# Kernel tuning notes

Measured on AMD Instinct MI355X. Metric: run time of the kernel, lower is better.

## Reference

```python
import jax, jax.numpy as jnp
import numpy as np

B, S, D, H = 2, 2048, 1024, 16
DK = D // H  # 64

def setup_inputs() -> dict:
    key = jax.random.key(0)
    ks = jax.random.split(key, 8)
    xavier = np.sqrt(6.0 / (D + D))  # xavier_uniform bound for square Linear
    def lin_w(k):
        return jax.random.uniform(k, (D, D), jnp.float32, -xavier, xavier)
    return {
        'Q': jax.random.normal(ks[0], (B, S, D), jnp.float32),
        'length': jax.random.randint(ks[1], (B,), 1, S + 1, jnp.int32),
        'Wq': lin_w(ks[2]), 'bq': jnp.zeros((D,), jnp.float32),
        'Wk': lin_w(ks[3]), 'bk': jnp.zeros((D,), jnp.float32),
        'Wv': lin_w(ks[4]), 'bv': jnp.zeros((D,), jnp.float32),
    }

def reference(Q, length, Wq, bq, Wk, bk, Wv, bv):
    # project and split heads: [B,S,D] -> [B,H,S,DK]
    def heads(x, W, b):
        y = jnp.einsum('bsd,de->bse', x, W) + b
        return y.reshape(B, S, H, DK).transpose(0, 2, 1, 3)
    q = heads(Q, Wq, bq)
    k = heads(Q, Wk, bk)
    v = heads(Q, Wv, bv)
    scores = jnp.einsum('bhqd,bhkd->bhqk', q, k) / np.sqrt(DK)
    scores = jnp.exp(scores)  # NOTE: raw exp, no max-subtraction (faithful)
    # multiplicative key mask: mask[b,k] = k < length[b], broadcast over q,h
    mask = (jnp.arange(S)[None, :] < length[:, None]).astype(scores.dtype)
    scores = scores * mask[:, None, None, :]
    attn = scores / (jnp.sum(scores, axis=-1, keepdims=True) + 1e-8)
    ctx = jnp.einsum('bhqk,bhkd->bhqd', attn, v)
    return ctx.transpose(0, 2, 1, 3).reshape(B, S, D)
```

## Files before the change

### kernel.cpp

```cpp
#include <hip/hip_runtime.h>
#include <hip/hip_bf16.h>

#define B_  2
#define S_  2048
#define D_  1024
#define H_  16
#define DK_ 64
#define M_  (B_ * S_)

typedef short short8 __attribute__((ext_vector_type(8)));
typedef float float4v __attribute__((ext_vector_type(4)));

#define QSCALE 0.18033688011112042f

static __device__ __forceinline__ ushort f32_to_bf16bits(float f) {
    union { __hip_bfloat16 h; ushort u; } cv;
    cv.h = __float2bfloat16(f);
    return cv.u;
}
static __device__ __forceinline__ unsigned pk2(float a, float b) {
    return (unsigned)f32_to_bf16bits(a) | ((unsigned)f32_to_bf16bits(b) << 16);
}

static __device__ __forceinline__ void glds16(const ushort* g, ushort* l) {
    __builtin_amdgcn_global_load_lds(
        (const __attribute__((address_space(1))) unsigned int*)g,
        (__attribute__((address_space(3))) unsigned int*)l, 16, 0, 0);
}

__global__ __launch_bounds__(256) void prep(
    const float* __restrict__ X, const float* __restrict__ W0,
    const float* __restrict__ W1, const float* __restrict__ W2,
    ushort* __restrict__ Xb, ushort* __restrict__ Wt)
{
    const int z = blockIdx.z;
    const int t = threadIdx.x;

    if (z >= 3) {
        const int blk = (z - 3) * 256 + blockIdx.y * 16 + blockIdx.x;
        const int i = blk * 2048 + t * 8;
        float4v a = *(const float4v*)(X + i);
        float4v b = *(const float4v*)(X + i + 4);
        short8 o;
        o[0] = (short)f32_to_bf16bits(a[0]); o[1] = (short)f32_to_bf16bits(a[1]);
        o[2] = (short)f32_to_bf16bits(a[2]); o[3] = (short)f32_to_bf16bits(a[3]);
        o[4] = (short)f32_to_bf16bits(b[0]); o[5] = (short)f32_to_bf16bits(b[1]);
        o[6] = (short)f32_to_bf16bits(b[2]); o[7] = (short)f32_to_bf16bits(b[3]);
        *(short8*)(Xb + i) = o;
        return;
    }

    const float* W = (z == 0) ? W0 : ((z == 1) ? W1 : W2);
    ushort* out = Wt + (size_t)z * D_ * D_;

    __shared__ ushort tile[64 * 72];
    int n0 = blockIdx.x * 64, k0 = blockIdx.y * 64;
    int r = t >> 3, g = t & 7;

    #pragma unroll
    for (int p = 0; p < 2; ++p) {
        int rr = r + p * 32;
        const float* src = W + (size_t)(k0 + rr) * D_ + n0 + g * 8;
        float4v a = *(const float4v*)src;
        float4v b = *(const float4v*)(src + 4);
        short8 o;
        o[0] = (short)f32_to_bf16bits(a[0]); o[1] = (short)f32_to_bf16bits(a[1]);
        o[2] = (short)f32_to_bf16bits(a[2]); o[3] = (short)f32_to_bf16bits(a[3]);
        o[4] = (short)f32_to_bf16bits(b[0]); o[5] = (short)f32_to_bf16bits(b[1]);
        o[6] = (short)f32_to_bf16bits(b[2]); o[7] = (short)f32_to_bf16bits(b[3]);
        *(short8*)&tile[rr * 72 + g * 8] = o;
    }
    __syncthreads();
    #pragma unroll
    for (int p = 0; p < 2; ++p) {
        int rr = r + p * 32;
        short8 v;
        #pragma unroll
        for (int i = 0; i < 8; ++i)
            v[i] = (short)tile[(g * 8 + i) * 72 + rr];
        *(short8*)(out + (size_t)(n0 + rr) * D_ + k0 + g * 8) = v;
    }
}

__global__ __launch_bounds__(256, 3) void proj_gemm(
    const ushort* __restrict__ X,
    const ushort* __restrict__ Wt,
    const float* __restrict__ b0, const float* __restrict__ b1,
    const float* __restrict__ b2,
    const int* __restrict__ length,
    ushort* __restrict__ qkv)
{
    const int z = blockIdx.z;
    const int m0 = blockIdx.x * 64, n0 = blockIdx.y * 128;

    if (z >= 1) {
        const int bidx = m0 >> 11;
        const int s0 = m0 & (S_ - 1);
        if (s0 >= length[bidx]) return;
    }

    const ushort* Wtz  = Wt + (size_t)z * D_ * D_;
    const float* bias = (z == 0) ? b0 : ((z == 1) ? b1 : b2);
    ushort* out = qkv + (size_t)z * M_ * D_;

    __shared__ __align__(16) ushort As[2][64 * 64];
    __shared__ __align__(16) ushort Bs[2][128 * 64];

    const int t = threadIdx.x;
    const int lane = t & 63, wid = t >> 6;
    const int quad = lane >> 4, l16 = lane & 15;
    const int wr = wid >> 1, wc = wid & 1;

    float4v acc[2][4] = {};

    #pragma unroll
    for (int j = 0; j < 2; ++j) {
        const int cid = wid * 128 + j * 64 + lane;
        const int row = cid >> 3;
        const int cl  = (cid & 7) ^ (row & 7);
        glds16(X + (size_t)(m0 + row) * D_ + cl * 8, &As[0][cid * 8]);
    }
    #pragma unroll
    for (int j = 0; j < 4; ++j) {
        const int cid = wid * 256 + j * 64 + lane;
        const int row = cid >> 3;
        const int cl  = (cid & 7) ^ (row & 7);
        glds16(Wtz + (size_t)(n0 + row) * D_ + cl * 8, &Bs[0][cid * 8]);
    }
    __syncthreads();

    for (int kt = 0; kt < 16; ++kt) {
        const int cur = kt & 1, nxt = cur ^ 1;
        if (kt + 1 < 16) {
            const int k0 = (kt + 1) * 64;
            #pragma unroll
            for (int j = 0; j < 2; ++j) {
                const int cid = wid * 128 + j * 64 + lane;
                const int row = cid >> 3;
                const int cl  = (cid & 7) ^ (row & 7);
                glds16(X + (size_t)(m0 + row) * D_ + k0 + cl * 8, &As[nxt][cid * 8]);
            }
            #pragma unroll
            for (int j = 0; j < 4; ++j) {
                const int cid = wid * 256 + j * 64 + lane;
                const int row = cid >> 3;
                const int cl  = (cid & 7) ^ (row & 7);
                glds16(Wtz + (size_t)(n0 + row) * D_ + k0 + cl * 8, &Bs[nxt][cid * 8]);
            }
        }

        #pragma unroll
        for (int ks = 0; ks < 2; ++ks) {
            short8 a[2], bb[4];
            #pragma unroll
            for (int i = 0; i < 2; ++i) {
                const int r = wr * 32 + i * 16 + l16;
                const int ph = (ks * 4 + quad) ^ (r & 7);
                a[i] = *(short8*)&As[cur][r * 64 + ph * 8];
            }
            #pragma unroll
            for (int j = 0; j < 4; ++j) {
                const int r = wc * 64 + j * 16 + l16;
                const int ph = (ks * 4 + quad) ^ (r & 7);
                bb[j] = *(short8*)&Bs[cur][r * 64 + ph * 8];
            }
            #pragma unroll
            for (int i = 0; i < 2; ++i)
                #pragma unroll
                for (int j = 0; j < 4; ++j)
                    acc[i][j] = __builtin_amdgcn_mfma_f32_16x16x32_bf16(
                        a[i], bb[j], acc[i][j], 0, 0, 0);
        }
        __syncthreads();
    }

    const float sc = (z == 0) ? QSCALE : 1.0f;
    #pragma unroll
    for (int j = 0; j < 4; ++j) {
        const int col = n0 + wc * 64 + j * 16 + l16;
        const float bv = bias[col];
        const int h = col >> 6, dk = col & (DK_ - 1);
        #pragma unroll
        for (int i = 0; i < 2; ++i) {
            #pragma unroll
            for (int rr = 0; rr < 4; ++rr) {
                const int row = m0 + wr * 32 + i * 16 + quad * 4 + rr;
                const int bidx = row >> 11;
                const int s = row & (S_ - 1);
                const float v = (acc[i][j][rr] + bv) * sc;
                size_t addr;
                if (z == 2)
                    addr = ((size_t)(bidx * H_ + h) * DK_ + dk) * S_ + s;
                else
                    addr = ((size_t)(bidx * H_ + h) * S_ + s) * DK_ + dk;
                out[addr] = f32_to_bf16bits(v);
            }
        }
    }
}

__global__ __launch_bounds__(256, 3) void attention(
    const ushort* __restrict__ qkv, const int* __restrict__ length,
    float* __restrict__ out)
{
    const int b = blockIdx.z, h = blockIdx.y, q0 = blockIdx.x * 64;
    int len = length[b];
    if (len > S_) len = S_;
    if (len < 1) len = 1;
    const int nkt = (len + 63) >> 6;

    const ushort* qb = qkv + ((size_t)(b * H_ + h) * S_ + q0) * DK_;
    const ushort* kb = qkv + (size_t)M_ * D_ + (size_t)(b * H_ + h) * S_ * DK_;
    const ushort* vb = qkv + (size_t)2 * M_ * D_ + (size_t)(b * H_ + h) * DK_ * S_;

    __shared__ __align__(16) ushort Qs[64 * 64];
    __shared__ __align__(16) ushort Ks[2][64 * 64];
    __shared__ __align__(16) ushort Vs[2][64 * 64];
    __shared__ __align__(16) ushort Ps[64 * 64];

    const int t = threadIdx.x, lane = t & 63, wid = t >> 6;
    const int quad = lane >> 4, l16 = lane & 15;
    const int qrow = wid * 16 + l16;
    const int e8 = (l16 & 7) << 1;

    #pragma unroll
    for (int j = 0; j < 2; ++j) {
        const int cid = wid * 128 + j * 64 + lane;
        const int row = cid >> 3;
        const int cl  = (cid & 7) ^ (row & 7);
        glds16(qb + (size_t)row * DK_ + cl * 8, &Qs[cid * 8]);
        glds16(kb + (size_t)row * DK_ + cl * 8, &Ks[0][cid * 8]);
        glds16(vb + (size_t)row * S_ + cl * 8,  &Vs[0][cid * 8]);
    }
    __syncthreads();

    float4v cacc[4] = {};
    float rs = 0.f;

    for (int kt = 0; kt < nkt; ++kt) {
        const int cur = kt & 1, nxt = cur ^ 1;
        if (kt + 1 < nkt) {
            #pragma unroll
            for (int j = 0; j < 2; ++j) {
                const int cid = wid * 128 + j * 64 + lane;
                const int row = cid >> 3;
                const int cl  = (cid & 7) ^ (row & 7);
                glds16(kb + (size_t)((kt + 1) * 64 + row) * DK_ + cl * 8,
                       &Ks[nxt][cid * 8]);
                glds16(vb + (size_t)row * S_ + (kt + 1) * 64 + cl * 8,
                       &Vs[nxt][cid * 8]);
            }
        }

        float4v sacc[4] = {};
        #pragma unroll
        for (int ks = 0; ks < 2; ++ks) {
            const int phb = (ks * 4 + quad) ^ (l16 & 7);
            short8 bq8 = *(short8*)&Qs[qrow * 64 + phb * 8];
            #pragma unroll
            for (int ct = 0; ct < 4; ++ct) {
                const int krow = ct * 16 + l16;
                const int pha = (ks * 4 + quad) ^ (krow & 7);
                short8 ak = *(short8*)&Ks[cur][krow * 64 + pha * 8];
                sacc[ct] = __builtin_amdgcn_mfma_f32_16x16x32_bf16(
                    ak, bq8, sacc[ct], 0, 0, 0);
            }
        }

        const bool full = ((kt + 1) * 64 <= len);
        #pragma unroll
        for (int ct = 0; ct < 4; ++ct) {
            float v0 = __builtin_amdgcn_exp2f(sacc[ct][0]);
            float v1 = __builtin_amdgcn_exp2f(sacc[ct][1]);
            float v2 = __builtin_amdgcn_exp2f(sacc[ct][2]);
            float v3 = __builtin_amdgcn_exp2f(sacc[ct][3]);
            if (!full) {
                const int kb0 = kt * 64 + ct * 16 + quad * 4;
                v0 = (kb0 + 0 < len) ? v0 : 0.f;
                v1 = (kb0 + 1 < len) ? v1 : 0.f;
                v2 = (kb0 + 2 < len) ? v2 : 0.f;
                v3 = (kb0 + 3 < len) ? v3 : 0.f;
            }
            rs += (v0 + v1) + (v2 + v3);
            uint2 w;
            w.x = pk2(v0, v1);
            w.y = pk2(v2, v3);
            const int c8 = (ct * 4 + quad) ^ e8;
            *(uint2*)&Ps[qrow * 64 + c8 * 4] = w;
        }

        #pragma unroll
        for (int ks = 0; ks < 2; ++ks) {
            const int pp = ((ks * 4 + quad) * 2) ^ e8;
            short8 ap = *(short8*)&Ps[qrow * 64 + pp * 4];
            #pragma unroll
            for (int ct = 0; ct < 4; ++ct) {
                const int vrow = ct * 16 + l16;
                const int phv = (ks * 4 + quad) ^ (vrow & 7);
                short8 vv = *(short8*)&Vs[cur][vrow * 64 + phv * 8];
                cacc[ct] = __builtin_amdgcn_mfma_f32_16x16x32_bf16(
                    ap, vv, cacc[ct], 0, 0, 0);
            }
        }
        __syncthreads();
    }

    rs += __shfl_xor(rs, 16);
    rs += __shfl_xor(rs, 32);

    #pragma unroll
    for (int rr = 0; rr < 4; ++rr) {
        const float rsq = __shfl(rs, quad * 4 + rr, 16);
        const float inv = 1.0f / (rsq + 1e-8f);
        const int q = q0 + wid * 16 + quad * 4 + rr;
        #pragma unroll
        for (int ct = 0; ct < 4; ++ct) {
            const int d = h * 64 + ct * 16 + l16;
            out[((size_t)b * S_ + q) * D_ + d] = cacc[ct][rr] * inv;
        }
    }
}

extern "C" void kernel_launch(void* const* d_in, const int* in_sizes, int n_in,
                              void* d_out, int out_size, void* d_ws, size_t ws_size,
                              hipStream_t stream)
{
    const float* Q   = (const float*)d_in[0];
    const int*   len = (const int*)d_in[1];
    const float* Wq  = (const float*)d_in[2];
    const float* bq  = (const float*)d_in[3];
    const float* Wk  = (const float*)d_in[4];
    const float* bk  = (const float*)d_in[5];
    const float* Wv  = (const float*)d_in[6];
    const float* bv  = (const float*)d_in[7];
    float* out = (float*)d_out;

    ushort* ws  = (ushort*)d_ws;
    ushort* Xb  = ws;
    ushort* Wt  = ws + (size_t)M_ * D_;
    ushort* qkv = Wt + (size_t)3 * D_ * D_;

    dim3 gPr(16, 16, 11);
    prep<<<gPr, 256, 0, stream>>>(Q, Wq, Wk, Wv, Xb, Wt);

    dim3 gP(M_ / 64, D_ / 128, 3);
    proj_gemm<<<gP, 256, 0, stream>>>(Xb, Wt, bq, bk, bv, len, qkv);

    dim3 gA(S_ / 64, H_, B_);
    attention<<<gA, 256, 0, stream>>>(qkv, len, out);
}
```

Before: 167.8 us.

## Fuse Q/K/V projections into one block sharing the X tile

The projection GEMM now computes the Q, K and V outputs in a single block, so each X tile is loaded into shared memory once and reused across all three weight matrices. The grid z dimension is removed, and the K/V work for masked rows is skipped with a per-block flag instead of an early return. In exchange, the double-buffered prefetch pipeline is dropped in favour of synchronous single-buffered loads. The larger B tile and three accumulator sets also raise shared memory and register use, and launch bounds drop to 2 blocks per SM. Blocks past the valid length now do only Q work while the others do triple work, which can cause load imbalance.

```diff
diff --git a/kernel.cpp b/kernel.cpp
--- a/kernel.cpp
+++ b/kernel.cpp
@@ -82,7 +82,7 @@
     }
 }
 
-__global__ __launch_bounds__(256, 3) void proj_gemm(
+__global__ __launch_bounds__(256, 2) void proj_gemm(
     const ushort* __restrict__ X,
     const ushort* __restrict__ Wt,
     const float* __restrict__ b0, const float* __restrict__ b1,
@@ -90,110 +90,109 @@
     const int* __restrict__ length,
     ushort* __restrict__ qkv)
 {
-    const int z = blockIdx.z;
     const int m0 = blockIdx.x * 64, n0 = blockIdx.y * 128;
-
-    if (z >= 1) {
-        const int bidx = m0 >> 11;
-        const int s0 = m0 & (S_ - 1);
-        if (s0 >= length[bidx]) return;
-    }
-
-    const ushort* Wtz  = Wt + (size_t)z * D_ * D_;
-    const float* bias = (z == 0) ? b0 : ((z == 1) ? b1 : b2);
-    ushort* out = qkv + (size_t)z * M_ * D_;
-
-    __shared__ __align__(16) ushort As[2][64 * 64];
-    __shared__ __align__(16) ushort Bs[2][128 * 64];
+    const int bidx = m0 >> 11;
+    const int s0 = m0 & (S_ - 1);
+    const bool kv = (s0 < length[bidx]);
+
+    __shared__ __align__(16) ushort As[64 * 64];
+    __shared__ __align__(16) ushort Bs[3][128 * 64];
 
     const int t = threadIdx.x;
     const int lane = t & 63, wid = t >> 6;
     const int quad = lane >> 4, l16 = lane & 15;
     const int wr = wid >> 1, wc = wid & 1;
 
-    float4v acc[2][4] = {};
-
-    #pragma unroll
-    for (int j = 0; j < 2; ++j) {
-        const int cid = wid * 128 + j * 64 + lane;
-        const int row = cid >> 3;
-        const int cl  = (cid & 7) ^ (row & 7);
-        glds16(X + (size_t)(m0 + row) * D_ + cl * 8, &As[0][cid * 8]);
-    }
-    #pragma unroll
-    for (int j = 0; j < 4; ++j) {
-        const int cid = wid * 256 + j * 64 + lane;
-        const int row = cid >> 3;
-        const int cl  = (cid & 7) ^ (row & 7);
-        glds16(Wtz + (size_t)(n0 + row) * D_ + cl * 8, &Bs[0][cid * 8]);
-    }
-    __syncthreads();
+    float4v accq[2][4] = {}, acck[2][4] = {}, accv[2][4] = {};
 
     for (int kt = 0; kt < 16; ++kt) {
-        const int cur = kt & 1, nxt = cur ^ 1;
-        if (kt + 1 < 16) {
-            const int k0 = (kt + 1) * 64;
-            #pragma unroll
-            for (int j = 0; j < 2; ++j) {
-                const int cid = wid * 128 + j * 64 + lane;
-                const int row = cid >> 3;
-                const int cl  = (cid & 7) ^ (row & 7);
-                glds16(X + (size_t)(m0 + row) * D_ + k0 + cl * 8, &As[nxt][cid * 8]);
-            }
-            #pragma unroll
-            for (int j = 0; j < 4; ++j) {
-                const int cid = wid * 256 + j * 64 + lane;
-                const int row = cid >> 3;
-                const int cl  = (cid & 7) ^ (row & 7);
-                glds16(Wtz + (size_t)(n0 + row) * D_ + k0 + cl * 8, &Bs[nxt][cid * 8]);
-            }
-        }
+        const int k0 = kt * 64;
+        __syncthreads();
+        #pragma unroll
+        for (int j = 0; j < 2; ++j) {
+            const int cid = wid * 128 + j * 64 + lane;
+            const int row = cid >> 3;
+            const int cl  = (cid & 7) ^ (row & 7);
+            glds16(X + (size_t)(m0 + row) * D_ + k0 + cl * 8, &As[cid * 8]);
+        }
+        #pragma unroll
+        for (int j = 0; j < 4; ++j) {
+            const int cid = wid * 256 + j * 64 + lane;
+            const int row = cid >> 3;
+            const int cl  = (cid & 7) ^ (row & 7);
+            const size_t off = (size_t)(n0 + row) * D_ + k0 + cl * 8;
+            glds16(Wt + off, &Bs[0][cid * 8]);
+            if (kv) {
+                glds16(Wt + (size_t)D_ * D_ + off,     &Bs[1][cid * 8]);
+                glds16(Wt + (size_t)2 * D_ * D_ + off, &Bs[2][cid * 8]);
+            }
+        }
+        __syncthreads();
 
         #pragma unroll
         for (int ks = 0; ks < 2; ++ks) {
-            short8 a[2], bb[4];
+            short8 a[2];
             #pragma unroll
             for (int i = 0; i < 2; ++i) {
                 const int r = wr * 32 + i * 16 + l16;
                 const int ph = (ks * 4 + quad) ^ (r & 7);
-                a[i] = *(short8*)&As[cur][r * 64 + ph * 8];
-            }
+                a[i] = *(short8*)&As[r * 64 + ph * 8];
+            }
+            short8 bq[4];
             #pragma unroll
             for (int j = 0; j < 4; ++j) {
                 const int r = wc * 64 + j * 16 + l16;
                 const int ph = (ks * 4 + quad) ^ (r & 7);
-                bb[j] = *(short8*)&Bs[cur][r * 64 + ph * 8];
+                bq[j] = *(short8*)&Bs[0][r * 64 + ph * 8];
             }
             #pragma unroll
             for (int i = 0; i < 2; ++i)
                 #pragma unroll
                 for (int j = 0; j < 4; ++j)
-                    acc[i][j] = __builtin_amdgcn_mfma_f32_16x16x32_bf16(
-                        a[i], bb[j], acc[i][j], 0, 0, 0);
-        }
-        __syncthreads();
-    }
-
-    const float sc = (z == 0) ? QSCALE : 1.0f;
+                    accq[i][j] = __builtin_amdgcn_mfma_f32_16x16x32_bf16(
+                        a[i], bq[j], accq[i][j], 0, 0, 0);
+            if (kv) {
+                short8 bk[4], bv[4];
+                #pragma unroll
+                for (int j = 0; j < 4; ++j) {
+                    const int r = wc * 64 + j * 16 + l16;
+                    const int ph = (ks * 4 + quad) ^ (r & 7);
+                    bk[j] = *(short8*)&Bs[1][r * 64 + ph * 8];
+                    bv[j] = *(short8*)&Bs[2][r * 64 + ph * 8];
+                }
+                #pragma unroll
+                for (int i = 0; i < 2; ++i)
+                    #pragma unroll
+                    for (int j = 0; j < 4; ++j) {
+                        acck[i][j] = __builtin_amdgcn_mfma_f32_16x16x32_bf16(
+                            a[i], bk[j], acck[i][j], 0, 0, 0);
+                        accv[i][j] = __builtin_amdgcn_mfma_f32_16x16x32_bf16(
+                            a[i], bv[j], accv[i][j], 0, 0, 0);
+                    }
+            }
+        }
+    }
+
     #pragma unroll
     for (int j = 0; j < 4; ++j) {
         const int col = n0 + wc * 64 + j * 16 + l16;
-        const float bv = bias[col];
         const int h = col >> 6, dk = col & (DK_ - 1);
+        const float bvq = b0[col], bvk = b1[col], bvv = b2[col];
         #pragma unroll
         for (int i = 0; i < 2; ++i) {
             #pragma unroll
             for (int rr = 0; rr < 4; ++rr) {
                 const int row = m0 + wr * 32 + i * 16 + quad * 4 + rr;
-                const int bidx = row >> 11;
                 const int s = row & (S_ - 1);
-                const float v = (acc[i][j][rr] + bv) * sc;
-                size_t addr;
-                if (z == 2)
-                    addr = ((size_t)(bidx * H_ + h) * DK_ + dk) * S_ + s;
-                else
-                    addr = ((size_t)(bidx * H_ + h) * S_ + s) * DK_ + dk;
-                out[addr] = f32_to_bf16bits(v);
+                const size_t hdr = ((size_t)(bidx * H_ + h) * S_ + s) * DK_ + dk;
+                qkv[hdr] = f32_to_bf16bits((accq[i][j][rr] + bvq) * QSCALE);
+                if (kv) {
+                    qkv[(size_t)M_ * D_ + hdr] =
+                        f32_to_bf16bits(acck[i][j][rr] + bvk);
+                    qkv[(size_t)2 * M_ * D_ +
+                        ((size_t)(bidx * H_ + h) * DK_ + dk) * S_ + s] =
+                        f32_to_bf16bits(accv[i][j][rr] + bvv);
+                }
             }
         }
     }
@@ -343,7 +342,7 @@
     dim3 gPr(16, 16, 11);
     prep<<<gPr, 256, 0, stream>>>(Q, Wq, Wk, Wv, Xb, Wt);
 
-    dim3 gP(M_ / 64, D_ / 128, 3);
+    dim3 gP(M_ / 64, D_ / 128);
     proj_gemm<<<gP, 256, 0, stream>>>(Xb, Wt, bq, bk, bv, len, qkv);
 
     dim3 gA(S_ / 64, H_, B_);
```

Result: faster. 157.2 us (-6.3%).
